# Kernel tuning notes

Measured on AMD Instinct MI355X. Metric: run time of the kernel, lower is better.

## Reference

```python
import jax, jax.numpy as jnp
import numpy as np

D_MODEL = 1024
HEADS = 16
D_K = D_MODEL // HEADS
D_FF = 4096
B, S = 2, 2048
EPS = 1e-5


def setup_inputs() -> dict:
    key = jax.random.key(0)
    ks = jax.random.split(key, 16)
    sc_att = 1.0 / np.sqrt(D_MODEL)
    sc_ff1 = 1.0 / np.sqrt(D_MODEL)
    sc_ff2 = 1.0 / np.sqrt(D_FF)
    return {
        "input": jax.random.normal(ks[0], (B, S, D_MODEL), jnp.float32),
        "mask": jnp.ones((B, 1, 1, S), jnp.int32),
        # stacked per-head projections: [H, D_MODEL, D_K]
        "Wq": jax.random.normal(ks[1], (HEADS, D_MODEL, D_K), jnp.float32) * sc_att,
        "bq": jax.random.normal(ks[2], (HEADS, D_K), jnp.float32) * 0.01,
        "Wk": jax.random.normal(ks[3], (HEADS, D_MODEL, D_K), jnp.float32) * sc_att,
        "bk": jax.random.normal(ks[4], (HEADS, D_K), jnp.float32) * 0.01,
        "Wv": jax.random.normal(ks[5], (HEADS, D_MODEL, D_K), jnp.float32) * sc_att,
        "bv": jax.random.normal(ks[6], (HEADS, D_K), jnp.float32) * 0.01,
        "Wo": jax.random.normal(ks[7], (D_MODEL, D_MODEL), jnp.float32) * sc_att,
        "bo": jax.random.normal(ks[8], (D_MODEL,), jnp.float32) * 0.01,
        "ln1_g": jnp.ones((D_MODEL,), jnp.float32),
        "ln1_b": jnp.zeros((D_MODEL,), jnp.float32),
        "ln2_g": jnp.ones((D_MODEL,), jnp.float32),
        "ln2_b": jnp.zeros((D_MODEL,), jnp.float32),
        "W1": jax.random.normal(ks[9], (D_MODEL, D_FF), jnp.float32) * sc_ff1,
        "b1": jax.random.normal(ks[10], (D_FF,), jnp.float32) * 0.01,
        "W2": jax.random.normal(ks[11], (D_FF, D_MODEL), jnp.float32) * sc_ff2,
        "b2": jax.random.normal(ks[12], (D_MODEL,), jnp.float32) * 0.01,
    }


def _layernorm(x, g, b):
    mu = jnp.mean(x, axis=-1, keepdims=True)
    var = jnp.mean(jnp.square(x - mu), axis=-1, keepdims=True)
    return (x - mu) * jax.lax.rsqrt(var + EPS) * g + b


def reference(input, mask, Wq, bq, Wk, bk, Wv, bv, Wo, bo,
              ln1_g, ln1_b, ln2_g, ln2_b, W1, b1, W2, b2):
    x = input
    # per-head projections, stacked: [B,H,S,D_K]
    q = jnp.einsum('bsd,hdk->bhsk', x, Wq) + bq[None, :, None, :]
    k = jnp.einsum('bsd,hdk->bhsk', x, Wk) + bk[None, :, None, :]
    v = jnp.einsum('bsd,hdk->bhsk', x, Wv) + bv[None, :, None, :]
    scores = jnp.einsum('bhqk,bhsk->bhqs', q, k) / np.sqrt(D_K)  # [B,H,S,S]
    scores = jnp.where(mask == 0, jnp.float32(-1e9), scores)
    attn = jax.nn.softmax(scores, axis=-1)
    ctx = jnp.einsum('bhqs,bhsk->bhqk', attn, v)  # [B,H,S,D_K]
    # concat heads along feature dim (head h occupies slice h*D_K:(h+1)*D_K)
    ctx = jnp.transpose(ctx, (0, 2, 1, 3)).reshape(B, S, D_MODEL)
    att_out = ctx @ Wo + bo
    h = _layernorm(x + att_out, ln1_g, ln1_b)
    ff = jax.nn.relu(h @ W1 + b1) @ W2 + b2
    return _layernorm(h + ff, ln2_g, ln2_b)
```

## Files before the change

### kernel.cpp

```cpp
#include <hip/hip_runtime.h>
#include <cstdint>
#include <cstddef>

typedef unsigned short u16;
typedef unsigned int   u32;
typedef unsigned short u16x4 __attribute__((ext_vector_type(4)));
typedef unsigned short u16x8 __attribute__((ext_vector_type(8)));
typedef unsigned int   u32x2 __attribute__((ext_vector_type(2)));
typedef unsigned int   u32x4 __attribute__((ext_vector_type(4)));
typedef __bf16 bf16x8 __attribute__((ext_vector_type(8)));
typedef float f32x4 __attribute__((ext_vector_type(4)));

#define MFMA16(a, b, c) __builtin_amdgcn_mfma_f32_16x16x32_bf16((a), (b), (c), 0, 0, 0)

__device__ __forceinline__ float bf2f(u16 h) {
  union { unsigned u; float f; } v; v.u = ((unsigned)h) << 16; return v.f;
}
__device__ __forceinline__ u16 f2bf(float f) {
  union { float f; unsigned u; } v; v.f = f;
  unsigned r = v.u + 0x7fffu + ((v.u >> 16) & 1u);
  return (u16)(r >> 16);
}
__device__ __forceinline__ u32 pack2(float a, float b) {
  union { float f; u32 u; } ua, ub; ua.f = a; ub.f = b;
  u32 ra = ua.u + 0x7fffu + ((ua.u >> 16) & 1u);
  u32 rb = ub.u + 0x7fffu + ((ub.u >> 16) & 1u);
  return __builtin_amdgcn_perm(rb, ra, 0x07060302);
}
__device__ __forceinline__ void gll16(const u16* g, u16* l) {
  __builtin_amdgcn_global_load_lds(
      (const __attribute__((address_space(1))) void*)g,
      (__attribute__((address_space(3))) void*)l, 16, 0, 0);
}
__device__ __forceinline__ float fast_exp2(float x) {
#if __has_builtin(__builtin_amdgcn_exp2f)
  return __builtin_amdgcn_exp2f(x);
#else
  return exp2f(x);
#endif
}
__device__ __forceinline__ void stage8(const float* g, u16* l) {
  float4 u = *(const float4*)g;
  float4 w = *(const float4*)(g + 4);
  u32x4 q;
  q[0] = pack2(u.x, u.y); q[1] = pack2(u.z, u.w);
  q[2] = pack2(w.x, w.y); q[3] = pack2(w.z, w.w);
  *(u32x4*)l = q;
}

__global__ __launch_bounds__(256) void transpose_qkv(
    const float* __restrict__ Wq, const float* __restrict__ Wk,
    const float* __restrict__ Wv, u16* __restrict__ outb) {
  __shared__ u16 tile[32][33];
  const int z = blockIdx.z;
  const int which = z >> 4, h = z & 15;
  const float* in = (which == 0 ? Wq : (which == 1 ? Wk : Wv)) + (size_t)h * 1024 * 64;
  u16* out = outb + ((size_t)which * 1024 + h * 64) * 1024;
  const int tx = threadIdx.x & 31, ty = threadIdx.x >> 5;
  const int r0 = blockIdx.y * 32, c0 = blockIdx.x * 32;
  #pragma unroll
  for (int i = 0; i < 32; i += 8)
    tile[ty + i][tx] = f2bf(in[(size_t)(r0 + ty + i) * 64 + c0 + tx]);
  __syncthreads();
  #pragma unroll
  for (int i = 0; i < 32; i += 8)
    out[(size_t)(c0 + ty + i) * 1024 + r0 + tx] = tile[tx][ty + i];
}

__global__ __launch_bounds__(256) void transpose_w(
    const float* __restrict__ Wo, const float* __restrict__ W1,
    const float* __restrict__ W2, u16* __restrict__ Wo_t,
    u16* __restrict__ W1_t, u16* __restrict__ W2_t) {
  __shared__ u16 tile[32][33];
  const int id = blockIdx.x;
  const float* in; u16* outp; int R, C, cx, ry;
  if (id < 1024)      { in = Wo; outp = Wo_t; R = 1024; C = 1024; cx = id & 31;  ry = id >> 5; }
  else if (id < 5120) { int t = id - 1024; in = W1; outp = W1_t; R = 1024; C = 4096; cx = t & 127; ry = t >> 7; }
  else                { int t = id - 5120; in = W2; outp = W2_t; R = 4096; C = 1024; cx = t & 31;  ry = t >> 5; }
  const int tx = threadIdx.x & 31, ty = threadIdx.x >> 5;
  const int r0 = ry * 32, c0 = cx * 32;
  #pragma unroll
  for (int i = 0; i < 32; i += 8)
    tile[ty + i][tx] = f2bf(in[(size_t)(r0 + ty + i) * C + c0 + tx]);
  __syncthreads();
  #pragma unroll
  for (int i = 0; i < 32; i += 8)
    outp[(size_t)(c0 + ty + i) * R + r0 + tx] = tile[tx][ty + i];
}

__global__ __launch_bounds__(256) void prep_small(
    const float* __restrict__ bq, const float* __restrict__ bk,
    const float* __restrict__ bv, const int* __restrict__ mask,
    float* __restrict__ biasq, float* __restrict__ madd2) {
  int i = blockIdx.x * 256 + threadIdx.x;
  if (i < 3072) {
    biasq[i] = (i < 1024) ? bq[i] : (i < 2048 ? bk[i - 1024] : bv[i - 2048]);
  } else if (i < 7168) {
    int j = i - 3072;
    madd2[j] = mask[j] ? -23.083120f : -1.442695e9f;
  }
}

template <int MODE, int AF32>
__global__ __launch_bounds__(256) void gemm_bt(
    const u16* __restrict__ A, const float* __restrict__ Af,
    const u16* __restrict__ Bt, const float* __restrict__ bias,
    u16* __restrict__ C, int M, int N, int K) {
  __shared__ __align__(16) u16 As[2][128 * 32];
  __shared__ __align__(16) u16 Bs[2][128 * 32];
  const int tid = threadIdx.x;
  const int lane = tid & 63;
  const int wave = tid >> 6;
  const int m0 = blockIdx.y * 128;
  const int n0 = blockIdx.x * 128;
  const int wr = (wave >> 1) * 64;
  const int wc = (wave & 1) * 64;
  const int lrow = lane & 15;
  const int quad = lane >> 4;

  const int srow = lane >> 2;
  const int scol = (lane & 3) * 8;
  const u16 *gA1 = nullptr, *gA2 = nullptr;
  const float *fA1 = nullptr, *fA2 = nullptr;
  if (AF32) {
    fA1 = &Af[(size_t)(m0 + wave * 16 + srow) * K + scol];
    fA2 = &Af[(size_t)(m0 + 64 + wave * 16 + srow) * K + scol];
  } else {
    gA1 = &A[(size_t)(m0 + wave * 16 + srow) * K + scol];
    gA2 = &A[(size_t)(m0 + 64 + wave * 16 + srow) * K + scol];
  }
  const u16* gB1 = &Bt[(size_t)(n0 + wave * 16 + srow) * K + scol];
  const u16* gB2 = &Bt[(size_t)(n0 + 64 + wave * 16 + srow) * K + scol];
  const int soA1 = (wave * 16 + srow) * 32 + scol;
  const int soA2 = (wave * 16 + 64 + srow) * 32 + scol;
  const int so1 = (wave * 16) * 32;
  const int so2 = (wave * 16 + 64) * 32;

  f32x4 acc[4][4];
  #pragma unroll
  for (int i = 0; i < 4; ++i)
    #pragma unroll
    for (int j = 0; j < 4; ++j)
      acc[i][j] = (f32x4){0.f, 0.f, 0.f, 0.f};

  for (int k0 = 0; k0 < K; k0 += 64) {
    if (AF32) {
      stage8(fA1 + k0,      &As[0][soA1]);
      stage8(fA2 + k0,      &As[0][soA2]);
      stage8(fA1 + k0 + 32, &As[1][soA1]);
      stage8(fA2 + k0 + 32, &As[1][soA2]);
    } else {
      gll16(gA1 + k0, &As[0][so1]);
      gll16(gA2 + k0, &As[0][so2]);
      gll16(gA1 + k0 + 32, &As[1][so1]);
      gll16(gA2 + k0 + 32, &As[1][so2]);
    }
    gll16(gB1 + k0, &Bs[0][so1]);
    gll16(gB2 + k0, &Bs[0][so2]);
    gll16(gB1 + k0 + 32, &Bs[1][so1]);
    gll16(gB2 + k0 + 32, &Bs[1][so2]);
    __syncthreads();
    #pragma unroll
    for (int kb = 0; kb < 2; ++kb) {
      bf16x8 af[4], bfr[4];
      #pragma unroll
      for (int i = 0; i < 4; ++i) {
        af[i]  = *(const bf16x8*)&As[kb][(wr + i * 16 + lrow) * 32 + quad * 8];
        bfr[i] = *(const bf16x8*)&Bs[kb][(wc + i * 16 + lrow) * 32 + quad * 8];
      }
      #pragma unroll
      for (int fr = 0; fr < 4; ++fr)
        #pragma unroll
        for (int fc = 0; fc < 4; ++fc)
          acc[fr][fc] = MFMA16(af[fr], bfr[fc], acc[fr][fc]);
    }
    __syncthreads();
  }

  #pragma unroll
  for (int fr = 0; fr < 4; ++fr) {
    int rowb = m0 + wr + fr * 16 + quad * 4;
    #pragma unroll
    for (int fc = 0; fc < 4; ++fc) {
      int col = n0 + wc + fc * 16 + lrow;
      float bv = bias[col];
      #pragma unroll
      for (int r = 0; r < 4; ++r) {
        float v = acc[fr][fc][r] + bv;
        if (MODE == 1) v = fmaxf(v, 0.f);
        C[(size_t)(rowb + r) * N + col] = f2bf(v);
      }
    }
  }
}

__global__ __launch_bounds__(256) void gemm64_bt(
    const u16* __restrict__ A, const u16* __restrict__ Bt,
    const float* __restrict__ bias, u16* __restrict__ C,
    int M, int N, int K) {
  __shared__ __align__(16) u16 As[2][64 * 32];
  __shared__ __align__(16) u16 Bs[2][128 * 32];
  const int tid = threadIdx.x;
  const int lane = tid & 63;
  const int wave = tid >> 6;
  const int m0 = blockIdx.y * 64;
  const int n0 = blockIdx.x * 128;
  const int wr = (wave >> 1) * 32;
  const int wc = (wave & 1) * 64;
  const int lrow = lane & 15;
  const int quad = lane >> 4;

  const int srow = lane >> 2;
  const int scol = (lane & 3) * 8;
  const u16* gA1 = &A[(size_t)(m0 + wave * 16 + srow) * K + scol];
  const u16* gB1 = &Bt[(size_t)(n0 + wave * 16 + srow) * K + scol];
  const u16* gB2 = &Bt[(size_t)(n0 + 64 + wave * 16 + srow) * K + scol];
  const int so1 = (wave * 16) * 32;
  const int so2 = (wave * 16 + 64) * 32;

  f32x4 acc[2][4];
  #pragma unroll
  for (int i = 0; i < 2; ++i)
    #pragma unroll
    for (int j = 0; j < 4; ++j)
      acc[i][j] = (f32x4){0.f, 0.f, 0.f, 0.f};

  for (int k0 = 0; k0 < K; k0 += 64) {
    gll16(gA1 + k0, &As[0][so1]);
    gll16(gB1 + k0, &Bs[0][so1]);
    gll16(gB2 + k0, &Bs[0][so2]);
    gll16(gA1 + k0 + 32, &As[1][so1]);
    gll16(gB1 + k0 + 32, &Bs[1][so1]);
    gll16(gB2 + k0 + 32, &Bs[1][so2]);
    __syncthreads();
    #pragma unroll
    for (int kb = 0; kb < 2; ++kb) {
      bf16x8 af[2], bfr[4];
      #pragma unroll
      for (int i = 0; i < 2; ++i)
        af[i] = *(const bf16x8*)&As[kb][(wr + i * 16 + lrow) * 32 + quad * 8];
      #pragma unroll
      for (int j = 0; j < 4; ++j)
        bfr[j] = *(const bf16x8*)&Bs[kb][(wc + j * 16 + lrow) * 32 + quad * 8];
      #pragma unroll
      for (int fr = 0; fr < 2; ++fr)
        #pragma unroll
        for (int fc = 0; fc < 4; ++fc)
          acc[fr][fc] = MFMA16(af[fr], bfr[fc], acc[fr][fc]);
    }
    __syncthreads();
  }

  #pragma unroll
  for (int fr = 0; fr < 2; ++fr) {
    int rowb = m0 + wr + fr * 16 + quad * 4;
    #pragma unroll
    for (int fc = 0; fc < 4; ++fc) {
      int col = n0 + wc + fc * 16 + lrow;
      float bv = bias[col];
      #pragma unroll
      for (int r = 0; r < 4; ++r) {
        float v = acc[fr][fc][r] + bv;
        C[(size_t)(rowb + r) * N + col] = f2bf(v);
      }
    }
  }
}

__global__ __launch_bounds__(256) void attn_kernel(
    const u16* __restrict__ xqkv, const float* __restrict__ madd2,
    u16* __restrict__ ctx) {
  __shared__ __align__(16) u16 Ks[64][72];
  __shared__ __align__(16) u16 Vt[64][136];
  __shared__ __align__(16) u16 Ps[4][2][16][72];
  const int tid = threadIdx.x;
  const int lane = tid & 63;
  const int wave = tid >> 6;
  const int lrow = lane & 15;
  const int quad = lane >> 4;
  const int b = blockIdx.z, h = blockIdx.y;
  const int qb = blockIdx.x * 128 + wave * 16;
  const u16* Qp = xqkv + (size_t)b * 2048 * 3072 + h * 64;
  const u16* Kp = Qp + 1024;
  const u16* Vp = Qp + 2048;
  const float S2 = 0.18033688f;

  bf16x8 qa[2][2];
  #pragma unroll
  for (int t = 0; t < 2; ++t) {
    qa[t][0] = *(const bf16x8*)&Qp[(size_t)(qb + t * 64 + lrow) * 3072 + quad * 8];
    qa[t][1] = *(const bf16x8*)&Qp[(size_t)(qb + t * 64 + lrow) * 3072 + 32 + quad * 8];
  }

  f32x4 o[2][4];
  #pragma unroll
  for (int t = 0; t < 2; ++t)
    #pragma unroll
    for (int i = 0; i < 4; ++i) o[t][i] = (f32x4){0.f, 0.f, 0.f, 0.f};
  float rsum[2] = {0.f, 0.f};

  const int ks_row = tid >> 3, ks_col = (tid & 7) * 8;
  const int v_dg = tid >> 4;
  const int v_kp = tid & 15;
  const float* maddb = madd2 + b * 2048;

  u16x8 kreg[2];
  u16x4 va[2], vb[2];
  #pragma unroll
  for (int sh = 0; sh < 2; ++sh) {
    kreg[sh] = *(const u16x8*)&Kp[(size_t)(sh * 32 + ks_row) * 3072 + ks_col];
    va[sh] = *(const u16x4*)&Vp[(size_t)(sh * 32 + 2 * v_kp) * 3072 + v_dg * 4];
    vb[sh] = *(const u16x4*)&Vp[(size_t)(sh * 32 + 2 * v_kp + 1) * 3072 + v_dg * 4];
  }

  for (int s0 = 0; s0 < 2048; s0 += 64) {
    __syncthreads();
    #pragma unroll
    for (int sh = 0; sh < 2; ++sh) {
      *(u16x8*)&Ks[sh * 32 + ks_row][ks_col] = kreg[sh];
      #pragma unroll
      for (int j = 0; j < 4; ++j) {
        u32 pk = ((u32)vb[sh][j] << 16) | (u32)va[sh][j];
        *(u32*)&Vt[v_dg * 4 + j][sh * 32 + 2 * v_kp] = pk;
      }
    }
    __syncthreads();
    if (s0 + 64 < 2048) {
      #pragma unroll
      for (int sh = 0; sh < 2; ++sh) {
        int sb = s0 + 64 + sh * 32;
        kreg[sh] = *(const u16x8*)&Kp[(size_t)(sb + ks_row) * 3072 + ks_col];
        va[sh] = *(const u16x4*)&Vp[(size_t)(sb + 2 * v_kp) * 3072 + v_dg * 4];
        vb[sh] = *(const u16x4*)&Vp[(size_t)(sb + 2 * v_kp + 1) * 3072 + v_dg * 4];
      }
    }

    bf16x8 kf[4][2], vf[4][2];
    #pragma unroll
    for (int kb = 0; kb < 4; ++kb) {
      kf[kb][0] = *(const bf16x8*)&Ks[kb * 16 + lrow][quad * 8];
      kf[kb][1] = *(const bf16x8*)&Ks[kb * 16 + lrow][32 + quad * 8];
    }
    #pragma unroll
    for (int nb = 0; nb < 4; ++nb) {
      vf[nb][0] = *(const bf16x8*)&Vt[nb * 16 + lrow][quad * 8];
      vf[nb][1] = *(const bf16x8*)&Vt[nb * 16 + lrow][32 + quad * 8];
    }

    #pragma unroll
    for (int t = 0; t < 2; ++t) {
      #pragma unroll
      for (int kb = 0; kb < 4; ++kb) {
        f32x4 z = (f32x4){0.f, 0.f, 0.f, 0.f};
        z = MFMA16(kf[kb][0], qa[t][0], z);
        z = MFMA16(kf[kb][1], qa[t][1], z);
        f32x4 m4 = *(const f32x4*)&maddb[s0 + kb * 16 + quad * 4];
        u32 pb[4];
        #pragma unroll
        for (int r = 0; r < 4; ++r) {
          float p = fast_exp2(fmaf(z[r], S2, m4[r]));
          rsum[t] += p;
          union { float f; u32 u; } cv; cv.f = p;
          pb[r] = cv.u + 0x8000u;
        }
        u32x2 w2;
        w2[0] = __builtin_amdgcn_perm(pb[1], pb[0], 0x07060302);
        w2[1] = __builtin_amdgcn_perm(pb[3], pb[2], 0x07060302);
        *(u32x2*)&Ps[wave][t][lrow][kb * 16 + quad * 4] = w2;
      }
      #pragma unroll
      for (int kh = 0; kh < 2; ++kh) {
        bf16x8 pa = *(const bf16x8*)&Ps[wave][t][lrow][kh * 32 + quad * 8];
        #pragma unroll
        for (int nb = 0; nb < 4; ++nb)
          o[t][nb] = MFMA16(pa, vf[nb][kh], o[t][nb]);
      }
    }
  }

  #pragma unroll
  for (int t = 0; t < 2; ++t) {
    float rs = rsum[t];
    rs += __shfl_xor(rs, 16, 64);
    rs += __shfl_xor(rs, 32, 64);
    float inv = 1.f / fmaxf(rs, 1e-30f);
    #pragma unroll
    for (int r = 0; r < 4; ++r) {
      float invq = __shfl(inv, quad * 4 + r, 64);
      int q = qb + t * 64 + quad * 4 + r;
      #pragma unroll
      for (int nb = 0; nb < 4; ++nb) {
        float v = o[t][nb][r] * invq;
        ctx[((size_t)b * 2048 + q) * 1024 + h * 64 + nb * 16 + lrow] = f2bf(v);
      }
    }
  }
}

template <int IN_BF, int OUT_BF>
__global__ __launch_bounds__(256) void add_ln(
    const void* __restrict__ xa_, const u16* __restrict__ ya,
    const float* __restrict__ g, const float* __restrict__ bb,
    void* __restrict__ outp_) {
  __shared__ float red[8];
  const int tid = threadIdx.x;
  const size_t base = (size_t)blockIdx.x * 1024;
  const float* xf = (const float*)xa_;
  const u16*   xb = (const u16*)xa_;
  float v[4];
  float s = 0.f;
  #pragma unroll
  for (int i = 0; i < 4; ++i) {
    int c = i * 256 + tid;
    float xv = IN_BF ? bf2f(xb[base + c]) : xf[base + c];
    v[i] = xv + bf2f(ya[base + c]);
    s += v[i];
  }
  #pragma unroll
  for (int off = 32; off > 0; off >>= 1) s += __shfl_down(s, off, 64);
  if ((tid & 63) == 0) red[tid >> 6] = s;
  __syncthreads();
  float mean = (red[0] + red[1] + red[2] + red[3]) * (1.f / 1024.f);
  float s2 = 0.f;
  #pragma unroll
  for (int i = 0; i < 4; ++i) { float d = v[i] - mean; s2 += d * d; }
  #pragma unroll
  for (int off = 32; off > 0; off >>= 1) s2 += __shfl_down(s2, off, 64);
  if ((tid & 63) == 0) red[4 + (tid >> 6)] = s2;
  __syncthreads();
  float var = (red[4] + red[5] + red[6] + red[7]) * (1.f / 1024.f);
  float rstd = rsqrtf(var + 1e-5f);
  #pragma unroll
  for (int i = 0; i < 4; ++i) {
    int c = i * 256 + tid;
    float r = (v[i] - mean) * rstd * g[c] + bb[c];
    if (OUT_BF) ((u16*)outp_)[base + c] = f2bf(r);
    else        ((float*)outp_)[base + c] = r;
  }
}

extern "C" void kernel_launch(void* const* d_in, const int* in_sizes, int n_in,
                              void* d_out, int out_size, void* d_ws, size_t ws_size,
                              hipStream_t stream) {
  (void)in_sizes; (void)n_in; (void)out_size; (void)ws_size;
  const float* x    = (const float*)d_in[0];
  const int*   mask = (const int*)d_in[1];
  const float* Wq   = (const float*)d_in[2];
  const float* bq   = (const float*)d_in[3];
  const float* Wk   = (const float*)d_in[4];
  const float* bk   = (const float*)d_in[5];
  const float* Wv   = (const float*)d_in[6];
  const float* bv   = (const float*)d_in[7];
  const float* Wo   = (const float*)d_in[8];
  const float* bo   = (const float*)d_in[9];
  const float* ln1g = (const float*)d_in[10];
  const float* ln1b = (const float*)d_in[11];
  const float* ln2g = (const float*)d_in[12];
  const float* ln2b = (const float*)d_in[13];
  const float* W1   = (const float*)d_in[14];
  const float* b1   = (const float*)d_in[15];
  const float* W2   = (const float*)d_in[16];
  const float* b2   = (const float*)d_in[17];
  float* out = (float*)d_out;

  char* ws = (char*)d_ws;
  u16*   Wqkv_t = (u16*)(ws + 0);
  u16*   Wo_t   = (u16*)(ws + 6291456);
  u16*   W1_t   = (u16*)(ws + 8388608);
  u16*   W2_t   = (u16*)(ws + 16777216);
  u16*   xqkv   = (u16*)(ws + 25165824);
  u16*   ctx    = (u16*)(ws + 50331648);
  u16*   ff1    = (u16*)(ws + 25165824);
  u16*   attout = (u16*)(ws + 58720256);
  u16*   ff2    = attout;
  u16*   hbuf   = (u16*)(ws + 67108864);
  float* biasq  = (float*)(ws + 75497472);
  float* madd2  = (float*)(ws + 75509760);

  prep_small<<<28, 256, 0, stream>>>(bq, bk, bv, mask, biasq, madd2);
  transpose_qkv<<<dim3(2, 32, 48), 256, 0, stream>>>(Wq, Wk, Wv, Wqkv_t);
  transpose_w<<<9216, 256, 0, stream>>>(Wo, W1, W2, Wo_t, W1_t, W2_t);

  gemm_bt<0, 1><<<dim3(24, 32), 256, 0, stream>>>(nullptr, x, Wqkv_t, biasq,
                                                  xqkv, 4096, 3072, 1024);
  attn_kernel<<<dim3(16, 16, 2), 256, 0, stream>>>(xqkv, madd2, ctx);
  gemm64_bt<<<dim3(8, 64), 256, 0, stream>>>(ctx, Wo_t, bo, attout, 4096, 1024, 1024);
  add_ln<0, 1><<<4096, 256, 0, stream>>>(x, attout, ln1g, ln1b, hbuf);
  gemm_bt<1, 0><<<dim3(32, 32), 256, 0, stream>>>(hbuf, nullptr, W1_t, b1,
                                                  ff1, 4096, 4096, 1024);
  gemm64_bt<<<dim3(8, 64), 256, 0, stream>>>(ff1, W2_t, b2, ff2, 4096, 1024, 4096);
  add_ln<1, 0><<<4096, 256, 0, stream>>>(hbuf, ff2, ln2g, ln2b, out);
}
```

Baseline: 406.2 us.

## Use split-K 128x128 GEMMs for N=1024 projections and pre-convert x to bf16

The two N=1024 GEMMs (output projection and FF2) move from 64x128 tiles to 128x128 tiles with a 2-way split over K. Each half writes a bf16 partial, and the add+layernorm kernel sums both partials and adds the bias. Separately, the fp32 input is converted to bf16 once in a new kernel, so the QKV GEMM can use direct global-to-LDS loads instead of in-loop fp32 staging and packing. This gives more data reuse per tile and keeps the block count equal, at the cost of extra partial traffic, an extra launch, and a small precision loss from rounding each partial to bf16.

Result: faster. 379.7 us (-6.5%).

```diff
diff --git a/kernel.cpp b/kernel.cpp
--- a/kernel.cpp
+++ b/kernel.cpp
@@ -7,7 +7,6 @@
 typedef unsigned short u16x4 __attribute__((ext_vector_type(4)));
 typedef unsigned short u16x8 __attribute__((ext_vector_type(8)));
 typedef unsigned int   u32x2 __attribute__((ext_vector_type(2)));
-typedef unsigned int   u32x4 __attribute__((ext_vector_type(4)));
 typedef __bf16 bf16x8 __attribute__((ext_vector_type(8)));
 typedef float f32x4 __attribute__((ext_vector_type(4)));
 
@@ -20,12 +19,6 @@
   union { float f; unsigned u; } v; v.f = f;
   unsigned r = v.u + 0x7fffu + ((v.u >> 16) & 1u);
   return (u16)(r >> 16);
-}
-__device__ __forceinline__ u32 pack2(float a, float b) {
-  union { float f; u32 u; } ua, ub; ua.f = a; ub.f = b;
-  u32 ra = ua.u + 0x7fffu + ((ua.u >> 16) & 1u);
-  u32 rb = ub.u + 0x7fffu + ((ub.u >> 16) & 1u);
-  return __builtin_amdgcn_perm(rb, ra, 0x07060302);
 }
 __device__ __forceinline__ void gll16(const u16* g, u16* l) {
   __builtin_amdgcn_global_load_lds(
@@ -38,14 +31,6 @@
 #else
   return exp2f(x);
 #endif
-}
-__device__ __forceinline__ void stage8(const float* g, u16* l) {
-  float4 u = *(const float4*)g;
-  float4 w = *(const float4*)(g + 4);
-  u32x4 q;
-  q[0] = pack2(u.x, u.y); q[1] = pack2(u.z, u.w);
-  q[2] = pack2(w.x, w.y); q[3] = pack2(w.z, w.w);
-  *(u32x4*)l = q;
 }
 
 __global__ __launch_bounds__(256) void transpose_qkv(
@@ -101,11 +86,21 @@
   }
 }
 
-template <int MODE, int AF32>
+__global__ __launch_bounds__(256) void cvt_x(
+    const float* __restrict__ in, u16* __restrict__ out, int n) {
+  int i = (blockIdx.x * 256 + threadIdx.x) * 4;
+  if (i >= n) return;
+  const float4 v = *(const float4*)&in[i];
+  u16x4 o;
+  o[0] = f2bf(v.x); o[1] = f2bf(v.y); o[2] = f2bf(v.z); o[3] = f2bf(v.w);
+  *(u16x4*)&out[i] = o;
+}
+
+template <int MODE>
 __global__ __launch_bounds__(256) void gemm_bt(
-    const u16* __restrict__ A, const float* __restrict__ Af,
-    const u16* __restrict__ Bt, const float* __restrict__ bias,
-    u16* __restrict__ C, int M, int N, int K) {
+    const u16* __restrict__ A, const u16* __restrict__ Bt,
+    const float* __restrict__ bias, u16* __restrict__ C,
+    int M, int N, int K) {
   __shared__ __align__(16) u16 As[2][128 * 32];
   __shared__ __align__(16) u16 Bs[2][128 * 32];
   const int tid = threadIdx.x;
@@ -120,19 +115,10 @@
 
   const int srow = lane >> 2;
   const int scol = (lane & 3) * 8;
-  const u16 *gA1 = nullptr, *gA2 = nullptr;
-  const float *fA1 = nullptr, *fA2 = nullptr;
-  if (AF32) {
-    fA1 = &Af[(size_t)(m0 + wave * 16 + srow) * K + scol];
-    fA2 = &Af[(size_t)(m0 + 64 + wave * 16 + srow) * K + scol];
-  } else {
-    gA1 = &A[(size_t)(m0 + wave * 16 + srow) * K + scol];
-    gA2 = &A[(size_t)(m0 + 64 + wave * 16 + srow) * K + scol];
-  }
+  const u16* gA1 = &A[(size_t)(m0 + wave * 16 + srow) * K + scol];
+  const u16* gA2 = &A[(size_t)(m0 + 64 + wave * 16 + srow) * K + scol];
   const u16* gB1 = &Bt[(size_t)(n0 + wave * 16 + srow) * K + scol];
   const u16* gB2 = &Bt[(size_t)(n0 + 64 + wave * 16 + srow) * K + scol];
-  const int soA1 = (wave * 16 + srow) * 32 + scol;
-  const int soA2 = (wave * 16 + 64 + srow) * 32 + scol;
   const int so1 = (wave * 16) * 32;
   const int so2 = (wave * 16 + 64) * 32;
 
@@ -144,19 +130,12 @@
       acc[i][j] = (f32x4){0.f, 0.f, 0.f, 0.f};
 
   for (int k0 = 0; k0 < K; k0 += 64) {
-    if (AF32) {
-      stage8(fA1 + k0,      &As[0][soA1]);
-      stage8(fA2 + k0,      &As[0][soA2]);
-      stage8(fA1 + k0 + 32, &As[1][soA1]);
-      stage8(fA2 + k0 + 32, &As[1][soA2]);
-    } else {
-      gll16(gA1 + k0, &As[0][so1]);
-      gll16(gA2 + k0, &As[0][so2]);
-      gll16(gA1 + k0 + 32, &As[1][so1]);
-      gll16(gA2 + k0 + 32, &As[1][so2]);
-    }
+    gll16(gA1 + k0, &As[0][so1]);
+    gll16(gA2 + k0, &As[0][so2]);
     gll16(gB1 + k0, &Bs[0][so1]);
     gll16(gB2 + k0, &Bs[0][so2]);
+    gll16(gA1 + k0 + 32, &As[1][so1]);
+    gll16(gA2 + k0 + 32, &As[1][so2]);
     gll16(gB1 + k0 + 32, &Bs[1][so1]);
     gll16(gB2 + k0 + 32, &Bs[1][so2]);
     __syncthreads();
@@ -194,56 +173,61 @@
   }
 }
 
-__global__ __launch_bounds__(256) void gemm64_bt(
+__global__ __launch_bounds__(256) void gemm_splitk(
     const u16* __restrict__ A, const u16* __restrict__ Bt,
-    const float* __restrict__ bias, u16* __restrict__ C,
-    int M, int N, int K) {
-  __shared__ __align__(16) u16 As[2][64 * 32];
+    u16* __restrict__ Cp, int M, int N, int K) {
+  __shared__ __align__(16) u16 As[2][128 * 32];
   __shared__ __align__(16) u16 Bs[2][128 * 32];
   const int tid = threadIdx.x;
   const int lane = tid & 63;
   const int wave = tid >> 6;
-  const int m0 = blockIdx.y * 64;
+  const int m0 = blockIdx.y * 128;
   const int n0 = blockIdx.x * 128;
-  const int wr = (wave >> 1) * 32;
+  const int kz = blockIdx.z;
+  const int Kh = K >> 1;
+  const int kbase = kz * Kh;
+  const int wr = (wave >> 1) * 64;
   const int wc = (wave & 1) * 64;
   const int lrow = lane & 15;
   const int quad = lane >> 4;
 
   const int srow = lane >> 2;
   const int scol = (lane & 3) * 8;
-  const u16* gA1 = &A[(size_t)(m0 + wave * 16 + srow) * K + scol];
-  const u16* gB1 = &Bt[(size_t)(n0 + wave * 16 + srow) * K + scol];
-  const u16* gB2 = &Bt[(size_t)(n0 + 64 + wave * 16 + srow) * K + scol];
+  const u16* gA1 = &A[(size_t)(m0 + wave * 16 + srow) * K + kbase + scol];
+  const u16* gA2 = &A[(size_t)(m0 + 64 + wave * 16 + srow) * K + kbase + scol];
+  const u16* gB1 = &Bt[(size_t)(n0 + wave * 16 + srow) * K + kbase + scol];
+  const u16* gB2 = &Bt[(size_t)(n0 + 64 + wave * 16 + srow) * K + kbase + scol];
   const int so1 = (wave * 16) * 32;
   const int so2 = (wave * 16 + 64) * 32;
-
-  f32x4 acc[2][4];
-  #pragma unroll
-  for (int i = 0; i < 2; ++i)
+  u16* C = Cp + (size_t)kz * M * N;
+
+  f32x4 acc[4][4];
+  #pragma unroll
+  for (int i = 0; i < 4; ++i)
     #pragma unroll
     for (int j = 0; j < 4; ++j)
       acc[i][j] = (f32x4){0.f, 0.f, 0.f, 0.f};
 
-  for (int k0 = 0; k0 < K; k0 += 64) {
+  for (int k0 = 0; k0 < Kh; k0 += 64) {
     gll16(gA1 + k0, &As[0][so1]);
+    gll16(gA2 + k0, &As[0][so2]);
     gll16(gB1 + k0, &Bs[0][so1]);
     gll16(gB2 + k0, &Bs[0][so2]);
     gll16(gA1 + k0 + 32, &As[1][so1]);
+    gll16(gA2 + k0 + 32, &As[1][so2]);
     gll16(gB1 + k0 + 32, &Bs[1][so1]);
     gll16(gB2 + k0 + 32, &Bs[1][so2]);
     __syncthreads();
     #pragma unroll
     for (int kb = 0; kb < 2; ++kb) {
-      bf16x8 af[2], bfr[4];
-      #pragma unroll
-      for (int i = 0; i < 2; ++i)
-        af[i] = *(const bf16x8*)&As[kb][(wr + i * 16 + lrow) * 32 + quad * 8];
-      #pragma unroll
-      for (int j = 0; j < 4; ++j)
-        bfr[j] = *(const bf16x8*)&Bs[kb][(wc + j * 16 + lrow) * 32 + quad * 8];
-      #pragma unroll
-      for (int fr = 0; fr < 2; ++fr)
+      bf16x8 af[4], bfr[4];
+      #pragma unroll
+      for (int i = 0; i < 4; ++i) {
+        af[i]  = *(const bf16x8*)&As[kb][(wr + i * 16 + lrow) * 32 + quad * 8];
+        bfr[i] = *(const bf16x8*)&Bs[kb][(wc + i * 16 + lrow) * 32 + quad * 8];
+      }
+      #pragma unroll
+      for (int fr = 0; fr < 4; ++fr)
         #pragma unroll
         for (int fc = 0; fc < 4; ++fc)
           acc[fr][fc] = MFMA16(af[fr], bfr[fc], acc[fr][fc]);
@@ -252,17 +236,14 @@
   }
 
   #pragma unroll
-  for (int fr = 0; fr < 2; ++fr) {
+  for (int fr = 0; fr < 4; ++fr) {
     int rowb = m0 + wr + fr * 16 + quad * 4;
     #pragma unroll
     for (int fc = 0; fc < 4; ++fc) {
       int col = n0 + wc + fc * 16 + lrow;
-      float bv = bias[col];
-      #pragma unroll
-      for (int r = 0; r < 4; ++r) {
-        float v = acc[fr][fc][r] + bv;
-        C[(size_t)(rowb + r) * N + col] = f2bf(v);
-      }
+      #pragma unroll
+      for (int r = 0; r < 4; ++r)
+        C[(size_t)(rowb + r) * N + col] = f2bf(acc[fr][fc][r]);
     }
   }
 }
@@ -398,8 +379,9 @@
 }
 
 template <int IN_BF, int OUT_BF>
-__global__ __launch_bounds__(256) void add_ln(
-    const void* __restrict__ xa_, const u16* __restrict__ ya,
+__global__ __launch_bounds__(256) void add_ln2p(
+    const void* __restrict__ xa_, const u16* __restrict__ p0,
+    const u16* __restrict__ p1, const float* __restrict__ cb,
     const float* __restrict__ g, const float* __restrict__ bb,
     void* __restrict__ outp_) {
   __shared__ float red[8];
@@ -413,7 +395,7 @@
   for (int i = 0; i < 4; ++i) {
     int c = i * 256 + tid;
     float xv = IN_BF ? bf2f(xb[base + c]) : xf[base + c];
-    v[i] = xv + bf2f(ya[base + c]);
+    v[i] = xv + bf2f(p0[base + c]) + bf2f(p1[base + c]) + cb[c];
     s += v[i];
   }
   #pragma unroll
@@ -465,14 +447,15 @@
 
   char* ws = (char*)d_ws;
   u16*   Wqkv_t = (u16*)(ws + 0);
+  u16*   fp     = (u16*)(ws + 0);
   u16*   Wo_t   = (u16*)(ws + 6291456);
   u16*   W1_t   = (u16*)(ws + 8388608);
   u16*   W2_t   = (u16*)(ws + 16777216);
   u16*   xqkv   = (u16*)(ws + 25165824);
+  u16*   wp     = (u16*)(ws + 25165824);
+  u16*   xb     = (u16*)(ws + 50331648);
   u16*   ctx    = (u16*)(ws + 50331648);
   u16*   ff1    = (u16*)(ws + 25165824);
-  u16*   attout = (u16*)(ws + 58720256);
-  u16*   ff2    = attout;
   u16*   hbuf   = (u16*)(ws + 67108864);
   float* biasq  = (float*)(ws + 75497472);
   float* madd2  = (float*)(ws + 75509760);
@@ -480,14 +463,17 @@
   prep_small<<<28, 256, 0, stream>>>(bq, bk, bv, mask, biasq, madd2);
   transpose_qkv<<<dim3(2, 32, 48), 256, 0, stream>>>(Wq, Wk, Wv, Wqkv_t);
   transpose_w<<<9216, 256, 0, stream>>>(Wo, W1, W2, Wo_t, W1_t, W2_t);
-
-  gemm_bt<0, 1><<<dim3(24, 32), 256, 0, stream>>>(nullptr, x, Wqkv_t, biasq,
-                                                  xqkv, 4096, 3072, 1024);
+  cvt_x<<<4096, 256, 0, stream>>>(x, xb, 4194304);
+
+  gemm_bt<0><<<dim3(24, 32), 256, 0, stream>>>(xb, Wqkv_t, biasq, xqkv,
+                                               4096, 3072, 1024);
   attn_kernel<<<dim3(16, 16, 2), 256, 0, stream>>>(xqkv, madd2, ctx);
-  gemm64_bt<<<dim3(8, 64), 256, 0, stream>>>(ctx, Wo_t, bo, attout, 4096, 1024, 1024);
-  add_ln<0, 1><<<4096, 256, 0, stream>>>(x, attout, ln1g, ln1b, hbuf);
-  gemm_bt<1, 0><<<dim3(32, 32), 256, 0, stream>>>(hbuf, nullptr, W1_t, b1,
-                                                  ff1, 4096, 4096, 1024);
-  gemm64_bt<<<dim3(8, 64), 256, 0, stream>>>(ff1, W2_t, b2, ff2, 4096, 1024, 4096);
-  add_ln<1, 0><<<4096, 256, 0, stream>>>(hbuf, ff2, ln2g, ln2b, out);
-}
+  gemm_splitk<<<dim3(8, 32, 2), 256, 0, stream>>>(ctx, Wo_t, wp, 4096, 1024, 1024);
+  add_ln2p<0, 1><<<4096, 256, 0, stream>>>(x, wp, wp + 4194304, bo,
+                                           ln1g, ln1b, hbuf);
+  gemm_bt<1><<<dim3(32, 32), 256, 0, stream>>>(hbuf, W1_t, b1, ff1,
+                                               4096, 4096, 1024);
+  gemm_splitk<<<dim3(8, 32, 2), 256, 0, stream>>>(ff1, W2_t, fp, 4096, 1024, 4096);
+  add_ln2p<1, 0><<<4096, 256, 0, stream>>>(hbuf, fp, fp + 4194304, b2,
+                                           ln2g, ln2b, out);
+}
```
